# Kernel tuning notes

Hardware: AMD Instinct MI355X
Metric: run time of the kernel (lower is better)

Reference implementation:

```python
import jax, jax.numpy as jnp
import numpy as np

FEAT_H = 32
FEAT_W = 32
GAUSS_THR = 0.6
GAUSS_3D_THR = 0.5
GAUSS_DEPTH_THR = 0.5
EXPAND = 1.2     # roi_expand_param
SIGMA = 1.6
BIN_OFFSET = 0.5
B, N, M = 4, 1024, 64


def setup_inputs() -> dict:
    key = jax.random.key(0)
    k1, k2, k3, k4, k5, k6, k7, k8, k9 = jax.random.split(key, 9)
    # ground-truth boxes inside a ~1024x768 image
    gx1 = jax.random.uniform(k1, (B, M)) * 800.0
    gy1 = jax.random.uniform(k2, (B, M)) * 600.0
    gw = jax.random.uniform(k3, (B, M)) * 200.0 + 32.0
    gh = jax.random.uniform(k4, (B, M)) * 200.0 + 32.0
    gt_box = jnp.stack([gx1, gy1, gx1 + gw, gy1 + gh], axis=-1)          # (B,M,4)
    # keypoint = (approx) box center, label in {0,1,2} (0 = ignore)
    kx = gx1 + 0.5 * gw + jax.random.normal(k5, (B, M)) * 2.0
    ky = gy1 + 0.5 * gh + jax.random.normal(k5, (B, M)) * 2.0
    klabel = jax.random.randint(k6, (B, M), 0, 3).astype(jnp.float32)
    dims = jax.random.uniform(k7, (B, M, 3)) * 3.0 + 0.5                 # l,h,w
    loc = jnp.concatenate([
        jax.random.normal(k8, (B, M, 2)) * 10.0,
        jax.random.uniform(k8, (B, M, 1)) * 75.0 + 5.0], axis=-1)       # x,y,depth
    rot = (jax.random.uniform(k9, (B, M, 1)) * 2.0 - 1.0) * np.pi
    gt_boxes = jnp.concatenate(
        [gt_box, kx[..., None], ky[..., None], klabel[..., None], dims, loc, rot],
        axis=-1).astype(jnp.float32)                                     # (B,M,14)
    match_gt_id = jax.random.randint(k2, (B, N), 0, M)
    matched4 = jnp.take_along_axis(gt_box, match_gt_id[..., None], axis=1)
    boxes = (matched4 + jax.random.normal(k3, (B, N, 4)) * 8.0).astype(jnp.float32)
    match_pos_flag = jax.random.randint(k4, (B, N), 0, 2).astype(jnp.int32)
    return {"boxes": boxes, "gt_boxes": gt_boxes,
            "match_pos_flag": match_pos_flag, "match_gt_id": match_gt_id}


def _forward(boxes, gt_boxes, match_pos_flag, match_gt_id):
    H, W = FEAT_H, FEAT_W
    dt = boxes.dtype
    # take_row: matched gt per proposal
    matched = jnp.take_along_axis(gt_boxes, match_gt_id[..., None], axis=1)  # (B,N,14)
    x1, y1, x2, y2 = (boxes[..., i] for i in range(4))
    # zoom_boxes: expand about center by roi_expand_param
    cx, cy = 0.5 * (x1 + x2), 0.5 * (y1 + y2)
    hw, hh = 0.5 * (x2 - x1) * EXPAND, 0.5 * (y2 - y1) * EXPAND
    ex1, ey1, ex2, ey2 = cx - hw, cy - hh, cx + hw, cy + hh
    sx = W / (ex2 - ex1 + 1.0)
    sy = H / (ey2 - ey1 + 1.0)
    kx = (matched[..., 4] - ex1) * sx                                    # (B,N)
    ky = (matched[..., 5] - ey1) * sy
    vis = matched[..., 6] != 0                                           # ignore_labels=(0,)
    valid = vis & (match_pos_flag > 0)                                   # (B,N)
    gx = jnp.arange(W, dtype=dt)[None, None, None, :]                    # bin x (cols)
    gy = jnp.arange(H, dtype=dt)[None, None, :, None]                    # bin y (rows)
    kxe, kye = kx[..., None, None], ky[..., None, None]
    two_sig2 = 2.0 * SIGMA * SIGMA
    score = jnp.exp(-(((gx + BIN_OFFSET - kxe) ** 2 +
                       (gy + BIN_OFFSET - kye) ** 2) / two_sig2))        # (B,N,H,W)
    offx = kxe - gx                                                      # (B,N,1,W), radius=1
    offy = kye - gy                                                      # (B,N,H,1)
    vmask = valid[..., None, None]
    m2 = (score >= GAUSS_THR) & vmask
    has = jnp.any(m2, axis=(-2, -1))                                     # (B,N) len(keep_pos)>0
    hasf = has[..., None, None].astype(dt)
    cls_label = jnp.where(has[..., None, None], score, -1.0)[:, :, None]           # (B,N,1,H,W)
    cls_label_w = jnp.broadcast_to(hasf, score.shape)[:, :, None]
    m2f = m2.astype(dt)
    reg_2d = jnp.stack([jnp.broadcast_to(offx * m2f, score.shape),
                        jnp.broadcast_to(offy * m2f, score.shape)], axis=2)         # (B,N,2,H,W)
    reg_2d_w = jnp.stack([m2f, m2f], axis=2)
    m3f = ((score >= GAUSS_3D_THR) & vmask).astype(dt)
    reg_3d = jnp.stack([jnp.broadcast_to(offx * m3f, score.shape),
                        jnp.broadcast_to(offy * m3f, score.shape)], axis=2)
    reg_3d_w = jnp.stack([m3f, m3f], axis=2)
    mdf = ((score >= GAUSS_DEPTH_THR) & vmask).astype(dt)
    depth = matched[..., 12][..., None, None]
    depth_label = (depth * mdf)[:, :, None]
    depth_label_w = mdf[:, :, None]
    dims = matched[..., 7:10]                                            # (B,N,3)
    dim_label = dims[..., None, None] * m3f[:, :, None]                  # (B,N,3,H,W)
    dim_label_w = jnp.broadcast_to(m3f[:, :, None], dim_label.shape)
    rot = matched[..., 13][..., None, None]
    rot_label = (rot * m3f)[:, :, None]
    rot_label_w = m3f[:, :, None]
    return (cls_label, cls_label_w, reg_2d, reg_2d_w, reg_3d, reg_3d_w,
            depth_label, depth_label_w, dim_label, dim_label_w,
            rot_label, rot_label_w)


def reference(boxes, gt_boxes, match_pos_flag, match_gt_id):
    return _forward(boxes, gt_boxes, match_pos_flag, match_gt_id)
```

## Files before the change

### kernel.cpp

```cpp
#include <hip/hip_runtime.h>

constexpr int B = 4, N = 1024, M = 64, H = 32, W = 32;
constexpr float EXPAND = 1.2f;
constexpr float TWO_SIG2 = 2.0f * 1.6f * 1.6f;
constexpr float GAUSS_THR = 0.6f;
constexpr float GAUSS_3D_THR = 0.5f;
constexpr int HW = H * W;
constexpr size_t S = (size_t)B * N * HW;


__global__ __launch_bounds__(256)
void rcnn3d_label_kernel(const float* __restrict__ boxes,
                         const float* __restrict__ gt_boxes,
                         const int*   __restrict__ pos_flag,
                         const int*   __restrict__ gt_id,
                         float* __restrict__ out)
{
    const int bn  = blockIdx.x;
    const int b   = bn >> 10;
    const int tid = threadIdx.x;

    const float4 bx = *reinterpret_cast<const float4*>(boxes + (size_t)bn * 4);
    const int   gid = gt_id[bn];
    const float* g  = gt_boxes + ((size_t)b * M + gid) * 14;
    const float kxg = g[4], kyg = g[5], klab = g[6];
    const float dim0 = g[7], dim1 = g[8], dim2 = g[9];
    const float depth = g[12], rot = g[13];
    const bool valid = (klab != 0.0f) && (pos_flag[bn] > 0);

    const float cx = 0.5f * (bx.x + bx.z);
    const float cy = 0.5f * (bx.y + bx.w);
    const float hw = 0.5f * (bx.z - bx.x) * EXPAND;
    const float hh = 0.5f * (bx.w - bx.y) * EXPAND;
    const float ex1 = cx - hw, ey1 = cy - hh;
    const float ex2 = cx + hw, ey2 = cy + hh;
    const float sx = (float)W / (ex2 - ex1 + 1.0f);
    const float sy = (float)H / (ey2 - ey1 + 1.0f);
    const float kx = (kxg - ex1) * sx;
    const float ky = (kyg - ey1) * sy;

    const int h  = tid >> 3;
    const int w0 = (tid & 7) * 4;
    const float gy   = (float)h;
    const float offy = ky - gy;
    const float dy   = gy + 0.5f - ky;
    const float dy2  = dy * dy;

    float score[4], offx[4];
    bool  m2[4], m3[4];
    bool  any2 = false;
#pragma unroll
    for (int j = 0; j < 4; ++j) {
        const float gx = (float)(w0 + j);
        const float dx = gx + 0.5f - kx;
        const float s  = expf(-((dx * dx + dy2) / TWO_SIG2));
        score[j] = s;
        offx[j]  = kx - gx;
        m2[j] = (s >= GAUSS_THR)    && valid;
        m3[j] = (s >= GAUSS_3D_THR) && valid;
        any2 |= m2[j];
    }

    __shared__ int s_has;
    if (tid == 0) s_has = 0;
    __syncthreads();
    if (any2) s_has = 1;
    __syncthreads();
    const bool has = (s_has != 0);

    float4 v_cls, v_clsw, v_rx2, v_ry2, v_w2, v_rx3, v_ry3, v_w3;
    float4 v_dep, v_d0, v_d1, v_d2, v_rot;
#pragma unroll
    for (int j = 0; j < 4; ++j) {
        const float f2 = m2[j] ? 1.0f : 0.0f;
        const float f3 = m3[j] ? 1.0f : 0.0f;
        (&v_cls.x)[j]  = has ? score[j] : -1.0f;
        (&v_clsw.x)[j] = has ? 1.0f : 0.0f;
        (&v_rx2.x)[j]  = offx[j] * f2;
        (&v_ry2.x)[j]  = offy    * f2;
        (&v_w2.x)[j]   = f2;
        (&v_rx3.x)[j]  = offx[j] * f3;
        (&v_ry3.x)[j]  = offy    * f3;
        (&v_w3.x)[j]   = f3;
        (&v_dep.x)[j]  = depth * f3;
        (&v_d0.x)[j]   = dim0 * f3;
        (&v_d1.x)[j]   = dim1 * f3;
        (&v_d2.x)[j]   = dim2 * f3;
        (&v_rot.x)[j]  = rot * f3;
    }

    const size_t cell = (size_t)tid * 4;
    const size_t bn1  = (size_t)bn * HW;
    const size_t bn2  = (size_t)bn * 2 * HW;
    const size_t bn3  = (size_t)bn * 3 * HW;
    auto st = [&](size_t ofs, const float4& v) {
        *reinterpret_cast<float4*>(out + ofs + cell) = v;
    };

    st( 0 * S + bn1,            v_cls);
    st( 1 * S + bn1,            v_clsw);
    st( 2 * S + bn2,            v_rx2);
    st( 2 * S + bn2 + HW,       v_ry2);
    st( 4 * S + bn2,            v_w2);
    st( 4 * S + bn2 + HW,       v_w2);
    st( 6 * S + bn2,            v_rx3);
    st( 6 * S + bn2 + HW,       v_ry3);
    st( 8 * S + bn2,            v_w3);
    st( 8 * S + bn2 + HW,       v_w3);
    st(10 * S + bn1,            v_dep);
    st(11 * S + bn1,            v_w3);
    st(12 * S + bn3,            v_d0);
    st(12 * S + bn3 + HW,       v_d1);
    st(12 * S + bn3 + 2 * HW,   v_d2);
    st(15 * S + bn3,            v_w3);
    st(15 * S + bn3 + HW,       v_w3);
    st(15 * S + bn3 + 2 * HW,   v_w3);
    st(18 * S + bn1,            v_rot);
    st(19 * S + bn1,            v_w3);
}

extern "C" void kernel_launch(void* const* d_in, const int* in_sizes, int n_in,
                              void* d_out, int out_size, void* d_ws, size_t ws_size,
                              hipStream_t stream) {
    const float* boxes    = (const float*)d_in[0];
    const float* gt_boxes = (const float*)d_in[1];
    const int*   pos_flag = (const int*)d_in[2];
    const int*   gt_id    = (const int*)d_in[3];
    float*       out      = (float*)d_out;

    rcnn3d_label_kernel<<<dim3(B * N), dim3(256), 0, stream>>>(
        boxes, gt_boxes, pos_flag, gt_id, out);
}
```

Before: 332.9 us.

## Split label generation into one block per output plane with nontemporal stores

The grid grows from one block per proposal to twenty blocks per proposal. Each block writes exactly one output plane, which gives fully contiguous per-block writes, and it stores them with nontemporal float4 stores. The per-proposal gaussian math and input loads are recomputed twenty times. The block-wide reduction and barrier now run only for the classification planes. The aim is to make the large write stream more sequential and to bypass cache, at the cost of redundant compute and more blocks.

```diff
diff --git a/kernel.cpp b/kernel.cpp
--- a/kernel.cpp
+++ b/kernel.cpp
@@ -1,32 +1,64 @@
 #include <hip/hip_runtime.h>
 
 constexpr int B = 4, N = 1024, M = 64, H = 32, W = 32;
-constexpr float EXPAND = 1.2f;
-constexpr float TWO_SIG2 = 2.0f * 1.6f * 1.6f;
-constexpr float GAUSS_THR = 0.6f;
-constexpr float GAUSS_3D_THR = 0.5f;
 constexpr int HW = H * W;
 constexpr size_t S = (size_t)B * N * HW;
+constexpr float EXPAND   = 1.2f;
+constexpr float TWO_SIG2 = 2.0f * 1.6f * 1.6f;
+constexpr float THR2 = 0.6f;
+constexpr float THR3 = 0.5f;
+
+typedef float vfloat4 __attribute__((ext_vector_type(4)));
 
 
 __global__ __launch_bounds__(256)
-void rcnn3d_label_kernel(const float* __restrict__ boxes,
+void rcnn3d_plane_kernel(const float* __restrict__ boxes,
                          const float* __restrict__ gt_boxes,
                          const int*   __restrict__ pos_flag,
                          const int*   __restrict__ gt_id,
                          float* __restrict__ out)
 {
-    const int bn  = blockIdx.x;
+    const int blk = blockIdx.x;
+    const int p   = blk >> 12;
+    const int bn  = blk & 4095;
     const int b   = bn >> 10;
     const int tid = threadIdx.x;
 
+    int mode, baseS, k, c;
+    switch (p) {
+        case 0:  mode=6; baseS=0;  k=1; c=0; break;
+        case 1:  mode=7; baseS=1;  k=1; c=0; break;
+        case 2:  mode=1; baseS=2;  k=2; c=0; break;
+        case 3:  mode=2; baseS=2;  k=2; c=1; break;
+        case 4:  mode=5; baseS=4;  k=2; c=0; break;
+        case 5:  mode=5; baseS=4;  k=2; c=1; break;
+        case 6:  mode=3; baseS=6;  k=2; c=0; break;
+        case 7:  mode=4; baseS=6;  k=2; c=1; break;
+        case 8:  mode=0; baseS=8;  k=2; c=0; break;
+        case 9:  mode=0; baseS=8;  k=2; c=1; break;
+        case 10: mode=0; baseS=10; k=1; c=0; break;
+        case 11: mode=0; baseS=11; k=1; c=0; break;
+        case 12: mode=0; baseS=12; k=3; c=0; break;
+        case 13: mode=0; baseS=12; k=3; c=1; break;
+        case 14: mode=0; baseS=12; k=3; c=2; break;
+        case 15: mode=0; baseS=15; k=3; c=0; break;
+        case 16: mode=0; baseS=15; k=3; c=1; break;
+        case 17: mode=0; baseS=15; k=3; c=2; break;
+        case 18: mode=0; baseS=18; k=1; c=0; break;
+        default: mode=0; baseS=19; k=1; c=0; break;
+    }
+
     const float4 bx = *reinterpret_cast<const float4*>(boxes + (size_t)bn * 4);
     const int   gid = gt_id[bn];
-    const float* g  = gt_boxes + ((size_t)b * M + gid) * 14;
-    const float kxg = g[4], kyg = g[5], klab = g[6];
-    const float dim0 = g[7], dim1 = g[8], dim2 = g[9];
-    const float depth = g[12], rot = g[13];
-    const bool valid = (klab != 0.0f) && (pos_flag[bn] > 0);
+    const float* g  = gt_boxes + ((size_t)b * 64 + gid) * 14;
+    const bool valid = (g[6] != 0.0f) && (pos_flag[bn] > 0);
+
+    float a = 1.0f;
+    if      (p == 10) a = g[12];
+    else if (p == 12) a = g[7];
+    else if (p == 13) a = g[8];
+    else if (p == 14) a = g[9];
+    else if (p == 18) a = g[13];
 
     const float cx = 0.5f * (bx.x + bx.z);
     const float cy = 0.5f * (bx.y + bx.w);
@@ -36,87 +68,62 @@
     const float ex2 = cx + hw, ey2 = cy + hh;
     const float sx = (float)W / (ex2 - ex1 + 1.0f);
     const float sy = (float)H / (ey2 - ey1 + 1.0f);
-    const float kx = (kxg - ex1) * sx;
-    const float ky = (kyg - ey1) * sy;
+    const float kx = (g[4] - ex1) * sx;
+    const float ky = (g[5] - ey1) * sy;
 
-    const int h  = tid >> 3;
-    const int w0 = (tid & 7) * 4;
-    const float gy   = (float)h;
+    const int hrow = tid >> 3;
+    const int w0   = (tid & 7) * 4;
+    const float gy   = (float)hrow;
     const float offy = ky - gy;
     const float dy   = gy + 0.5f - ky;
     const float dy2  = dy * dy;
 
-    float score[4], offx[4];
-    bool  m2[4], m3[4];
+    float s4[4], ox4[4];
+    bool  m2v[4], m3v[4];
     bool  any2 = false;
 #pragma unroll
     for (int j = 0; j < 4; ++j) {
         const float gx = (float)(w0 + j);
         const float dx = gx + 0.5f - kx;
         const float s  = expf(-((dx * dx + dy2) / TWO_SIG2));
-        score[j] = s;
-        offx[j]  = kx - gx;
-        m2[j] = (s >= GAUSS_THR)    && valid;
-        m3[j] = (s >= GAUSS_3D_THR) && valid;
-        any2 |= m2[j];
+        s4[j]  = s;
+        ox4[j] = kx - gx;
+        m2v[j] = (s >= THR2) && valid;
+        m3v[j] = (s >= THR3) && valid;
+        any2  |= m2v[j];
     }
 
-    __shared__ int s_has;
-    if (tid == 0) s_has = 0;
-    __syncthreads();
-    if (any2) s_has = 1;
-    __syncthreads();
-    const bool has = (s_has != 0);
+    bool has = false;
+    if (mode >= 6) {
+        __shared__ int s_has;
+        if (tid == 0) s_has = 0;
+        __syncthreads();
+        if (any2) s_has = 1;
+        __syncthreads();
+        has = (s_has != 0);
+    }
 
-    float4 v_cls, v_clsw, v_rx2, v_ry2, v_w2, v_rx3, v_ry3, v_w3;
-    float4 v_dep, v_d0, v_d1, v_d2, v_rot;
+    vfloat4 v;
 #pragma unroll
     for (int j = 0; j < 4; ++j) {
-        const float f2 = m2[j] ? 1.0f : 0.0f;
-        const float f3 = m3[j] ? 1.0f : 0.0f;
-        (&v_cls.x)[j]  = has ? score[j] : -1.0f;
-        (&v_clsw.x)[j] = has ? 1.0f : 0.0f;
-        (&v_rx2.x)[j]  = offx[j] * f2;
-        (&v_ry2.x)[j]  = offy    * f2;
-        (&v_w2.x)[j]   = f2;
-        (&v_rx3.x)[j]  = offx[j] * f3;
-        (&v_ry3.x)[j]  = offy    * f3;
-        (&v_w3.x)[j]   = f3;
-        (&v_dep.x)[j]  = depth * f3;
-        (&v_d0.x)[j]   = dim0 * f3;
-        (&v_d1.x)[j]   = dim1 * f3;
-        (&v_d2.x)[j]   = dim2 * f3;
-        (&v_rot.x)[j]  = rot * f3;
+        const float f2 = m2v[j] ? 1.0f : 0.0f;
+        const float f3 = m3v[j] ? 1.0f : 0.0f;
+        float val;
+        switch (mode) {
+            case 0:  val = a * f3;               break;
+            case 1:  val = ox4[j] * f2;          break;
+            case 2:  val = offy * f2;            break;
+            case 3:  val = ox4[j] * f3;          break;
+            case 4:  val = offy * f3;            break;
+            case 5:  val = f2;                   break;
+            case 6:  val = has ? s4[j] : -1.0f;  break;
+            default: val = has ? 1.0f : 0.0f;    break;
+        }
+        v[j] = val;
     }
 
-    const size_t cell = (size_t)tid * 4;
-    const size_t bn1  = (size_t)bn * HW;
-    const size_t bn2  = (size_t)bn * 2 * HW;
-    const size_t bn3  = (size_t)bn * 3 * HW;
-    auto st = [&](size_t ofs, const float4& v) {
-        *reinterpret_cast<float4*>(out + ofs + cell) = v;
-    };
-
-    st( 0 * S + bn1,            v_cls);
-    st( 1 * S + bn1,            v_clsw);
-    st( 2 * S + bn2,            v_rx2);
-    st( 2 * S + bn2 + HW,       v_ry2);
-    st( 4 * S + bn2,            v_w2);
-    st( 4 * S + bn2 + HW,       v_w2);
-    st( 6 * S + bn2,            v_rx3);
-    st( 6 * S + bn2 + HW,       v_ry3);
-    st( 8 * S + bn2,            v_w3);
-    st( 8 * S + bn2 + HW,       v_w3);
-    st(10 * S + bn1,            v_dep);
-    st(11 * S + bn1,            v_w3);
-    st(12 * S + bn3,            v_d0);
-    st(12 * S + bn3 + HW,       v_d1);
-    st(12 * S + bn3 + 2 * HW,   v_d2);
-    st(15 * S + bn3,            v_w3);
-    st(15 * S + bn3 + HW,       v_w3);
-    st(15 * S + bn3 + 2 * HW,   v_w3);
-    st(18 * S + bn1,            v_rot);
-    st(19 * S + bn1,            v_w3);
+    float* dst = out + (size_t)baseS * S + ((size_t)bn * k + c) * HW + (size_t)tid * 4;
+    __builtin_nontemporal_store(v, reinterpret_cast<vfloat4*>(dst));
 }
 
 extern "C" void kernel_launch(void* const* d_in, const int* in_sizes, int n_in,
@@ -128,6 +135,6 @@
     const int*   gt_id    = (const int*)d_in[3];
     float*       out      = (float*)d_out;
 
-    rcnn3d_label_kernel<<<dim3(B * N), dim3(256), 0, stream>>>(
+    rcnn3d_plane_kernel<<<dim3(20 * 4096), dim3(256), 0, stream>>>(
         boxes, gt_boxes, pos_flag, gt_id, out);
 }
```

Result: slower. 371.4 us (+11.6%).
